# Optimization experiments

Measured on AMD Instinct MI355X. Metric: run time of the kernel, lower is better.

Reference implementation:

```python
import jax, jax.numpy as jnp
import numpy as np
from jax import lax

# 4D convolution via lax.conv_general_dilated (supports N spatial dims natively)
# Layout: x is (N, C, T, U, V, W); weight is (O, I, kT, kU, kV, kW)

def conv4d(x, w, b):
    dn = lax.conv_dimension_numbers(x.shape, w.shape, ('NCTUVW', 'OITUVW', 'NCTUVW'))
    y = lax.conv_general_dilated(x, w, window_strides=(1, 1, 1, 1), padding='SAME',
                                 dimension_numbers=dn)
    return y + b[None, :, None, None, None, None]


def setup_inputs() -> dict:
    key = jax.random.key(0)
    k0, k1, k2, k3, k4 = jax.random.split(key, 5)
    B, C_in, C_hid, C_out = 2, 64, 128, 64
    T, D, H, W = 4, 16, 32, 32
    K = 3  # kernel size per dim (stmode 'C' -> (3,3,3,3))
    x = jax.random.normal(k0, (B, C_in, T, D, H, W), dtype=jnp.float32)
    scale1 = 1.0 / np.sqrt(C_in * K ** 4)
    scale2 = 1.0 / np.sqrt(C_hid * K ** 4)
    w1 = jax.random.normal(k1, (C_hid, C_in, K, K, K, K), dtype=jnp.float32) * scale1
    b1 = jax.random.normal(k2, (C_hid,), dtype=jnp.float32) * scale1
    w2 = jax.random.normal(k3, (C_out, C_hid, K, K, K, K), dtype=jnp.float32) * scale2
    b2 = jax.random.normal(k4, (C_out,), dtype=jnp.float32) * scale2
    return {"x": x, "w1": w1, "b1": b1, "w2": w2, "b2": b2}


def reference(x, w1, b1, w2, b2):
    # conv1 -> ReLU -> (dropout p=0 is identity) -> conv2 -> (dropout identity)
    h = jax.nn.relu(conv4d(x, w1, b1))
    return conv4d(h, w2, b2)
```

## Files before the change

kernel.cpp:

```cpp
#include <hip/hip_runtime.h>


using bf16x8 = __attribute__((ext_vector_type(8))) __bf16;
using f32x16 = __attribute__((ext_vector_type(16))) float;
using f32x4  = __attribute__((ext_vector_type(4))) float;

typedef __attribute__((address_space(1))) const void as1_void;
typedef __attribute__((address_space(3))) void as3_void;
__device__ __forceinline__ void gload_lds16(const void* g, void* l) {
    __builtin_amdgcn_global_load_lds((as1_void*)g, (as3_void*)l, 16, 0, 0);
}

__global__ __launch_bounds__(256) void cvt_x(const float* __restrict__ x,
                                             __bf16* __restrict__ x_t,
                                             __bf16* __restrict__ zp) {
    __shared__ float lt[64][65];
    if (blockIdx.x == 0 && blockIdx.y == 0)
        *(uint4*)((char*)zp + threadIdx.x * 16) = make_uint4(0u, 0u, 0u, 0u);
    const int nb = blockIdx.y;
    const int p0 = blockIdx.x * 64;
    const int tu = p0 >> 10;
    const float* src = x + (size_t)nb * 64 * 65536;
    __bf16* dst = x_t + (size_t)nb * 65536 * 64;
    #pragma unroll
    for (int i = 0; i < 16; ++i) {
        int idx = i * 256 + threadIdx.x;
        int c = idx >> 6, p = idx & 63;
        lt[c][p] = src[(size_t)c * 65536 + p0 + p];
    }
    __syncthreads();
    #pragma unroll
    for (int it = 0; it < 2; ++it) {
        int idx = it * 256 + threadIdx.x;
        int pl = idx & 63;
        int chunk = idx >> 6;
        int p = p0 + pl;
        int v = (p >> 5) & 31, w = p & 31;
        bf16x8 pk;
        #pragma unroll
        for (int e = 0; e < 8; ++e)
            pk[e] = (__bf16)lt[chunk * 8 + e][pl];
        *(bf16x8*)(dst + (size_t)(tu * 32 + v) * 2048 + chunk * 256 + w * 8) = pk;
    }
}

template <int CIN>
__global__ __launch_bounds__(256) void cvt_w(const float* __restrict__ w,
                                             __bf16* __restrict__ wt) {
    constexpr int COUT = 8192 / CIN;
    constexpr int LOGC = (CIN == 64) ? 7 : 6;
    const int tap = blockIdx.x;
    __bf16* dst = wt + (size_t)tap * 8192;
    #pragma unroll
    for (int it = 0; it < 32; ++it) {
        const int i  = it * 256 + threadIdx.x;
        const int cl = i & 15;
        const int o  = (i >> 4) & (COUT - 1);
        const int kg = i >> (4 + LOGC);
        dst[i] = (__bf16)w[(size_t)(o * CIN + kg * 16 + cl) * 81 + tap];
    }
}

template <int CIN, int COUT, int NSPLIT, bool RELU>
__global__ __launch_bounds__(128, 2) void conv4d_mfma(
    const __bf16* __restrict__ in_t,
    const __bf16* __restrict__ wt,
    const float* __restrict__ bias,
    __bf16* __restrict__ out_bf,
    float* __restrict__ out_f,
    const __bf16* __restrict__ zpage)
{
    constexpr int KST     = CIN / 16;
    constexpr int UNITS   = CIN / 32;
    constexpr int LOGU    = (UNITS == 2) ? 1 : 2;
    constexpr int SLOTS   = 6 * 136;
    constexpr int SLOTS_P = 896;
    constexpr int RNDS    = 7;
    constexpr int BUFB_P  = SLOTS_P * 16;

    __shared__ __bf16 tile[2 * SLOTS_P * 8];

    const int tid  = threadIdx.x;
    const int lane = tid & 63;
    const int l31  = lane & 31;
    const int hl   = lane >> 5;
    const int wv   = tid >> 6;

    const int bid = blockIdx.x;
    const int xcd = bid & 7;
    const int s0  = bid >> 3;
    const int u   = xcd * 2 + (s0 & 1);
    const int vg  = (s0 >> 1) & 7;
    const int t   = (s0 >> 4) & 3;
    const int nb  = (s0 >> 6) & 1;
    const int nsp = (s0 >> 7) & (NSPLIT - 1);
    const int v0  = vg * 4;
    const int pbase = ((t * 16 + u) * 32 + v0) * 32;

    const __bf16* inb = in_t + (size_t)nb * 65536 * CIN;

    int goff[RNDS];
    #pragma unroll
    for (int r = 0; r < RNDS; ++r) {
        const int slot = r * 128 + tid;
        const int row  = slot / 136;
        const int rem  = slot - row * 136;
        const int chunk = rem / 34;
        const int wp   = rem - chunk * 34;
        const int v_in = v0 - 1 + row;
        const int w_in = wp - 1;
        const bool ok = (slot < SLOTS) && ((unsigned)v_in < 32u) &&
                        ((unsigned)w_in < 32u);
        goff[r] = ok ? (v_in * (CIN * 32) + chunk * 256 + w_in * 8) : -1;
    }

    const int lane_base = hl * 34 + l31;
    const bf16x8* tile16 = (const bf16x8*)tile;

    const int o = nsp * 64 + wv * 32 + l31;
    const __bf16* wlane = wt + (size_t)o * 16 + hl * 8;

    int sb[9], tb0[9], nst = 0;
    #pragma unroll
    for (int kt = 0; kt < 3; ++kt) {
        const int t_in = t + kt - 1;
        if ((unsigned)t_in >= 4u) continue;
        #pragma unroll
        for (int ku = 0; ku < 3; ++ku) {
            const int u_in = u + ku - 1;
            if ((unsigned)u_in >= 16u) continue;
            sb[nst]  = (t_in * 16 + u_in) * 1024 * CIN;
            tb0[nst] = (kt * 3 + ku) * 9;
            ++nst;
        }
    }
    const int U = nst * UNITS;

    f32x16 acc[4];
    #pragma unroll
    for (int mt = 0; mt < 4; ++mt)
        #pragma unroll
        for (int i = 0; i < 16; ++i)
            acc[mt][i] = 0.f;

    auto issue = [&](int buf, int j) {
        const int st = j >> LOGU, ch = j & (UNITS - 1);
        const __bf16* gb = inb + sb[st] + ch * 1024;
        char* lb = ((char*)tile) + buf * BUFB_P + wv * 1024;
        #pragma unroll
        for (int r = 0; r < RNDS; ++r) {
            const __bf16* ga = (goff[r] >= 0) ? gb + goff[r] : zpage;
            gload_lds16(ga, lb + r * 2048);
        }
    };

    auto ldA = [&](const bf16x8* tb, int g, bf16x8 (&af)[6]) {
        const int ks = g / 3, kw = g % 3;
        #pragma unroll
        for (int j = 0; j < 6; ++j)
            af[j] = tb[j * 136 + ks * 68 + kw];
    };
    auto ldB = [&](int tapb, int ch, int g, bf16x8 (&bv)[3]) {
        const int ks = g / 3, kw = g % 3;
        const int ksg = ch * 2 + ks;
        #pragma unroll
        for (int kv = 0; kv < 3; ++kv) {
            const int wo = ((tapb + kv * 3 + kw) * KST + ksg) * (COUT * 16);
            bv[kv] = *(const bf16x8*)(wlane + wo);
        }
    };
    auto mfma12 = [&](bf16x8 (&af)[6], bf16x8 (&bv)[3]) {
        __builtin_amdgcn_s_setprio(1);
        #pragma unroll
        for (int kv = 0; kv < 3; ++kv)
            #pragma unroll
            for (int rr = 0; rr < 4; ++rr)
                acc[rr] = __builtin_amdgcn_mfma_f32_32x32x16_bf16(
                    af[rr + kv], bv[kv], acc[rr], 0, 0, 0);
        __builtin_amdgcn_s_setprio(0);
    };

    issue(0, 0);
    bf16x8 bv[6][3];
    #pragma unroll
    for (int g = 0; g < 6; ++g)
        ldB(tb0[0], 0, g, bv[g]);

    #pragma unroll 1
    for (int i = 0; i < U; ++i) {
        asm volatile("s_waitcnt vmcnt(18)" ::: "memory");
        __builtin_amdgcn_s_barrier();
        __builtin_amdgcn_sched_barrier(0);

        const bool more = (i + 1 < U);
        const int nu = more ? i + 1 : i;
        issue((i + 1) & 1, nu);
        __builtin_amdgcn_sched_barrier(0);

        const int ntapb = tb0[nu >> LOGU];
        const int nch   = nu & (UNITS - 1);
        const bf16x8* tb = tile16 + (i & 1) * SLOTS_P + lane_base;

        bf16x8 afA[6], afB[6], afC[6];
        ldA(tb, 0, afA);
        ldA(tb, 1, afB);
        ldA(tb, 2, afC);
        mfma12(afA, bv[0]); ldA(tb, 3, afA); ldB(ntapb, nch, 0, bv[0]);
        mfma12(afB, bv[1]); ldA(tb, 4, afB); ldB(ntapb, nch, 1, bv[1]);
        mfma12(afC, bv[2]); ldA(tb, 5, afC); ldB(ntapb, nch, 2, bv[2]);
        mfma12(afA, bv[3]); ldB(ntapb, nch, 3, bv[3]);
        mfma12(afB, bv[4]); ldB(ntapb, nch, 4, bv[4]);
        mfma12(afC, bv[5]); ldB(ntapb, nch, 5, bv[5]);
    }

    {
        const float bvls = bias[o];
        #pragma unroll
        for (int rr = 0; rr < 4; ++rr) {
            const int pb = pbase + rr * 32;
            if constexpr (RELU) {
                #pragma unroll
                for (int rg = 0; rg < 4; ++rg)
                    #pragma unroll
                    for (int j = 0; j < 4; ++j) {
                        float v = acc[rr][rg * 4 + j] + bvls;
                        v = v > 0.f ? v : 0.f;
                        const int p = pb + j + 8 * rg + 4 * hl;
                        const int vv = (p >> 5) & 31, ww = p & 31, tu = p >> 10;
                        out_bf[(size_t)nb * 65536 * COUT +
                               (size_t)(tu * 32 + vv) * (32 * COUT) +
                               (o >> 3) * 256 + ww * 8 + (o & 7)] = (__bf16)v;
                    }
            } else {
                #pragma unroll
                for (int rg = 0; rg < 4; ++rg) {
                    f32x4 sv;
                    #pragma unroll
                    for (int j = 0; j < 4; ++j)
                        sv[j] = acc[rr][rg * 4 + j] + bvls;
                    const int p = pb + 8 * rg + 4 * hl;
                    *(f32x4*)(out_f + ((size_t)nb * COUT + o) * 65536 + p) = sv;
                }
            }
        }
    }
}

extern "C" void kernel_launch(void* const* d_in, const int* in_sizes, int n_in,
                              void* d_out, int out_size, void* d_ws, size_t ws_size,
                              hipStream_t stream) {
    const float* x  = (const float*)d_in[0];
    const float* w1 = (const float*)d_in[1];
    const float* b1 = (const float*)d_in[2];
    const float* w2 = (const float*)d_in[3];
    const float* b2 = (const float*)d_in[4];
    float* out = (float*)d_out;

    char* ws = (char*)d_ws;
    __bf16* x_t = (__bf16*)ws;
    __bf16* h_t = (__bf16*)(ws + 16777216);
    __bf16* w1t = (__bf16*)(ws + 50331648);
    __bf16* w2t = (__bf16*)(ws + 51658752);
    __bf16* zpg = (__bf16*)(ws + 52985856);

    cvt_x<<<dim3(1024, 2), 256, 0, stream>>>(x, x_t, zpg);
    cvt_w<64><<<81, 256, 0, stream>>>(w1, w1t);
    cvt_w<128><<<81, 256, 0, stream>>>(w2, w2t);

    conv4d_mfma<64, 128, 2, true><<<2048, 128, 0, stream>>>(x_t, w1t, b1, h_t,
                                                            nullptr, zpg);
    conv4d_mfma<128, 64, 1, false><<<1024, 128, 0, stream>>>(h_t, w2t, b2,
                                                             nullptr, out, zpg);
}
```

Measured before the change: 383.1 us.

## Drop cross-iteration B-weight prefetch and setprio, load weights at loop top

Removes the software pipelining that prefetched the next unit's weight fragments during the MFMA chain. Each iteration now waits for all outstanding loads (vmcnt(0)), loads the current unit's weights up front, then issues the next tile copy. It also shrinks the A-fragment buffers from three to two and drops the s_setprio wrapping around the MFMAs. This lowers register pressure, which may help occupancy or avoid spills. The cost is that global weight-load latency is no longer hidden behind compute and the full vmcnt(0) wait serialises each iteration.

```diff
diff --git a/kernel.cpp b/kernel.cpp
--- a/kernel.cpp
+++ b/kernel.cpp
@@ -170,47 +170,46 @@
         }
     };
     auto mfma12 = [&](bf16x8 (&af)[6], bf16x8 (&bv)[3]) {
-        __builtin_amdgcn_s_setprio(1);
         #pragma unroll
         for (int kv = 0; kv < 3; ++kv)
             #pragma unroll
             for (int rr = 0; rr < 4; ++rr)
                 acc[rr] = __builtin_amdgcn_mfma_f32_32x32x16_bf16(
                     af[rr + kv], bv[kv], acc[rr], 0, 0, 0);
-        __builtin_amdgcn_s_setprio(0);
     };
 
     issue(0, 0);
-    bf16x8 bv[6][3];
-    #pragma unroll
-    for (int g = 0; g < 6; ++g)
-        ldB(tb0[0], 0, g, bv[g]);
 
     #pragma unroll 1
     for (int i = 0; i < U; ++i) {
-        asm volatile("s_waitcnt vmcnt(18)" ::: "memory");
+        asm volatile("s_waitcnt vmcnt(0)" ::: "memory");
         __builtin_amdgcn_s_barrier();
+
+        const int st = i >> LOGU, ch = i & (UNITS - 1);
+        const int tapb = tb0[st];
+        const bf16x8* tb = tile16 + (i & 1) * SLOTS_P + lane_base;
+
+        bf16x8 bvv[6][3];
+        #pragma unroll
+        for (int g = 0; g < 6; ++g)
+            ldB(tapb, ch, g, bvv[g]);
         __builtin_amdgcn_sched_barrier(0);
-
-        const bool more = (i + 1 < U);
-        const int nu = more ? i + 1 : i;
-        issue((i + 1) & 1, nu);
+        if (i + 1 < U) issue((i + 1) & 1, i + 1);
         __builtin_amdgcn_sched_barrier(0);
 
-        const int ntapb = tb0[nu >> LOGU];
-        const int nch   = nu & (UNITS - 1);
-        const bf16x8* tb = tile16 + (i & 1) * SLOTS_P + lane_base;
-
-        bf16x8 afA[6], afB[6], afC[6];
+        bf16x8 afA[6], afB[6];
         ldA(tb, 0, afA);
         ldA(tb, 1, afB);
-        ldA(tb, 2, afC);
-        mfma12(afA, bv[0]); ldA(tb, 3, afA); ldB(ntapb, nch, 0, bv[0]);
-        mfma12(afB, bv[1]); ldA(tb, 4, afB); ldB(ntapb, nch, 1, bv[1]);
-        mfma12(afC, bv[2]); ldA(tb, 5, afC); ldB(ntapb, nch, 2, bv[2]);
-        mfma12(afA, bv[3]); ldB(ntapb, nch, 3, bv[3]);
-        mfma12(afB, bv[4]); ldB(ntapb, nch, 4, bv[4]);
-        mfma12(afC, bv[5]); ldB(ntapb, nch, 5, bv[5]);
+        mfma12(afA, bvv[0]);
+        ldA(tb, 2, afA);
+        mfma12(afB, bvv[1]);
+        ldA(tb, 3, afB);
+        mfma12(afA, bvv[2]);
+        ldA(tb, 4, afA);
+        mfma12(afB, bvv[3]);
+        ldA(tb, 5, afB);
+        mfma12(afA, bvv[4]);
+        mfma12(afB, bvv[5]);
     }
 
     {
```

Result: faster. 374.1 us (-2.4%).

## Split weight prefetch into halves with inline-asm loads and explicit vmcnt waits

Applied to the files above, without the earlier changes.

The conv main loop now loads B (weight) fragments through inline-asm global loads in two halves of nine registers. The second half is loaded just-in-time at the top of each iteration, and the first half for the next unit is prefetched mid-iteration. Explicit vmcnt waits order these loads against the LDS tile DMA. A-fragment loads are interleaved one group at a time with the MFMAs, and the s_setprio hints are dropped. The aim is to cut register pressure and control load/compute overlap by hand. In exchange, the loop now waits on vmcnt(0) at the top of every iteration, which may expose weight-load latency.

```diff
diff --git a/kernel.cpp b/kernel.cpp
--- a/kernel.cpp
+++ b/kernel.cpp
@@ -10,6 +10,12 @@
 __device__ __forceinline__ void gload_lds16(const void* g, void* l) {
     __builtin_amdgcn_global_load_lds((as1_void*)g, (as3_void*)l, 16, 0, 0);
 }
+__device__ __forceinline__ bf16x8 gload16(const __bf16* p) {
+    bf16x8 r;
+    asm volatile("global_load_dwordx4 %0, %1, off" : "=v"(r) : "v"(p));
+    return r;
+}
+#define SBAR() __builtin_amdgcn_sched_barrier(0)
 
 __global__ __launch_bounds__(256) void cvt_x(const float* __restrict__ x,
                                              __bf16* __restrict__ x_t,
@@ -160,58 +166,79 @@
         for (int j = 0; j < 6; ++j)
             af[j] = tb[j * 136 + ks * 68 + kw];
     };
-    auto ldB = [&](int tapb, int ch, int g, bf16x8 (&bv)[3]) {
+    auto ldB3 = [&](int tapb, int ch, int g, bf16x8* dst) {
         const int ks = g / 3, kw = g % 3;
         const int ksg = ch * 2 + ks;
         #pragma unroll
         for (int kv = 0; kv < 3; ++kv) {
             const int wo = ((tapb + kv * 3 + kw) * KST + ksg) * (COUT * 16);
-            bv[kv] = *(const bf16x8*)(wlane + wo);
+            dst[kv] = gload16(wlane + wo);
         }
     };
-    auto mfma12 = [&](bf16x8 (&af)[6], bf16x8 (&bv)[3]) {
-        __builtin_amdgcn_s_setprio(1);
-        #pragma unroll
-        for (int kv = 0; kv < 3; ++kv)
-            #pragma unroll
-            for (int rr = 0; rr < 4; ++rr)
-                acc[rr] = __builtin_amdgcn_mfma_f32_32x32x16_bf16(
-                    af[rr + kv], bv[kv], acc[rr], 0, 0, 0);
-        __builtin_amdgcn_s_setprio(0);
+    auto mfma12 = [&](bf16x8 (&af)[6], const bf16x8& b0, const bf16x8& b1,
+                      const bf16x8& b2) {
+        #pragma unroll
+        for (int rr = 0; rr < 4; ++rr)
+            acc[rr] = __builtin_amdgcn_mfma_f32_32x32x16_bf16(af[rr + 0], b0,
+                                                              acc[rr], 0, 0, 0);
+        #pragma unroll
+        for (int rr = 0; rr < 4; ++rr)
+            acc[rr] = __builtin_amdgcn_mfma_f32_32x32x16_bf16(af[rr + 1], b1,
+                                                              acc[rr], 0, 0, 0);
+        #pragma unroll
+        for (int rr = 0; rr < 4; ++rr)
+            acc[rr] = __builtin_amdgcn_mfma_f32_32x32x16_bf16(af[rr + 2], b2,
+                                                              acc[rr], 0, 0, 0);
     };
 
     issue(0, 0);
-    bf16x8 bv[6][3];
-    #pragma unroll
-    for (int g = 0; g < 6; ++g)
-        ldB(tb0[0], 0, g, bv[g]);
+    bf16x8 bvF[9], bvS[9];
+    #pragma unroll
+    for (int g = 0; g < 3; ++g)
+        ldB3(tb0[0], 0, g, &bvF[g * 3]);
 
     #pragma unroll 1
     for (int i = 0; i < U; ++i) {
-        asm volatile("s_waitcnt vmcnt(18)" ::: "memory");
+        asm volatile("s_waitcnt vmcnt(0)" ::: "memory");
         __builtin_amdgcn_s_barrier();
-        __builtin_amdgcn_sched_barrier(0);
-
+        SBAR();
+
+        const int st = i >> LOGU, ch = i & (UNITS - 1);
+        const int tapb = tb0[st];
         const bool more = (i + 1 < U);
         const int nu = more ? i + 1 : i;
-        issue((i + 1) & 1, nu);
-        __builtin_amdgcn_sched_barrier(0);
-
         const int ntapb = tb0[nu >> LOGU];
         const int nch   = nu & (UNITS - 1);
         const bf16x8* tb = tile16 + (i & 1) * SLOTS_P + lane_base;
 
-        bf16x8 afA[6], afB[6], afC[6];
-        ldA(tb, 0, afA);
-        ldA(tb, 1, afB);
-        ldA(tb, 2, afC);
-        mfma12(afA, bv[0]); ldA(tb, 3, afA); ldB(ntapb, nch, 0, bv[0]);
-        mfma12(afB, bv[1]); ldA(tb, 4, afB); ldB(ntapb, nch, 1, bv[1]);
-        mfma12(afC, bv[2]); ldA(tb, 5, afC); ldB(ntapb, nch, 2, bv[2]);
-        mfma12(afA, bv[3]); ldB(ntapb, nch, 3, bv[3]);
-        mfma12(afB, bv[4]); ldB(ntapb, nch, 4, bv[4]);
-        mfma12(afC, bv[5]); ldB(ntapb, nch, 5, bv[5]);
-    }
+        #pragma unroll
+        for (int g = 0; g < 3; ++g)
+            ldB3(tapb, ch, g + 3, &bvS[g * 3]);
+        SBAR();
+        issue((i + 1) & 1, nu);
+        SBAR();
+
+        bf16x8 af[6];
+        ldA(tb, 0, af); mfma12(af, bvF[0], bvF[1], bvF[2]);
+        ldA(tb, 1, af); mfma12(af, bvF[3], bvF[4], bvF[5]);
+        ldA(tb, 2, af); mfma12(af, bvF[6], bvF[7], bvF[8]);
+        #pragma unroll
+        for (int g = 0; g < 3; ++g)
+            ldB3(ntapb, nch, g, &bvF[g * 3]);
+        SBAR();
+        asm volatile("s_waitcnt vmcnt(16)" ::: "memory");
+        SBAR();
+        ldA(tb, 3, af); mfma12(af, bvS[0], bvS[1], bvS[2]);
+        ldA(tb, 4, af); mfma12(af, bvS[3], bvS[4], bvS[5]);
+        ldA(tb, 5, af); mfma12(af, bvS[6], bvS[7], bvS[8]);
+    }
+
+    asm volatile("s_waitcnt vmcnt(0)" ::: "memory");
+    SBAR();
+    asm volatile("" ::
+        "v"(bvF[0]), "v"(bvF[1]), "v"(bvF[2]), "v"(bvF[3]), "v"(bvF[4]),
+        "v"(bvF[5]), "v"(bvF[6]), "v"(bvF[7]), "v"(bvF[8]));
+    SBAR();
 
     {
         const float bvls = bias[o];
```

New measurement: 389.5 us. About the same (+1.6%).
